# Optimization experiments

Hardware: AMD Instinct MI355X
Metric: run time of the kernel (lower is better)

## Reference

```python
import jax, jax.numpy as jnp
import numpy as np

B, N, C, E, K = 2, 1024, 128, 64, 20

def setup_inputs() -> dict:
    key = jax.random.key(0)
    ks = jax.random.split(key, 4)
    x = jax.random.normal(ks[0], (B, N, C), dtype=jnp.float32)
    Wl = jax.random.normal(ks[1], (C, E), dtype=jnp.float32) * 0.05
    Wr = jax.random.normal(ks[2], (C, E), dtype=jnp.float32) * 0.05
    att = jax.random.normal(ks[3], (1, E), dtype=jnp.float32) * 0.1
    bl = jnp.zeros((E,), dtype=jnp.float32)
    br = jnp.zeros((E,), dtype=jnp.float32)
    edge_index = jnp.zeros((2, 1), dtype=jnp.int64)
    batch = jnp.zeros((B * N,), dtype=jnp.int64)
    return {"x": x, "Wl": Wl, "bl": bl, "Wr": Wr, "br": br, "att": att,
            "edge_index": edge_index, "batch": batch}

def reference(x, Wl, bl, Wr, br, att, edge_index, batch):
    # x: [B, N, C]
    b, n, _ = x.shape
    x_l = x @ Wl + bl              # [B, N, E]
    x_r = x @ Wr + br              # [B, N, E]
    # dense pairwise scores: leaky_relu(x_l_i + x_r_j) . att  -> [B, N, N]
    x_cat = jax.nn.leaky_relu(x_l[:, :, None, :] + x_r[:, None, :, :], 0.2)
    alpha = jnp.einsum('bijd,d->bij', x_cat, att[0])
    alpha = jnp.nan_to_num(alpha, nan=0.0, posinf=0.0, neginf=0.0)
    k = min(K, n)
    vals, idx = jax.lax.top_k(alpha, k)            # [B, N, k]
    attention = jax.nn.softmax(vals, axis=-1).reshape(-1)  # [B*N*k]
    # edge index construction (dropout p used only in training; eval = identity)
    offset = (jnp.arange(b) * n)[:, None]                      # [B, 1]
    index_i = jnp.tile(jnp.repeat(jnp.arange(n), k)[None, :], (b, 1)) + offset
    index_j = idx.reshape(b, n * k) + offset
    new_edge_index = jnp.stack([index_i.reshape(-1), index_j.reshape(-1)], axis=0)
    return new_edge_index, attention
```

## Files before the change

kernel.cpp:

```cpp
#include <hip/hip_runtime.h>

#define Bq 2
#define Nq 1024
#define Cq 128
#define Eq 64
#define Kq 20
#define TI 4
#define BN (Bq * Nq)
#define BNK (BN * Kq)
#define NEGF (-3.0e38f)

#define DPP_F(x, ctrl) __int_as_float(__builtin_amdgcn_update_dpp( \
    __float_as_int(x), __float_as_int(x), (ctrl), 0xf, 0xf, false))
#define DPP_I(x, ctrl) __builtin_amdgcn_update_dpp((x), (x), (ctrl), 0xf, 0xf, false)
#define RL_F(x, l) __int_as_float(__builtin_amdgcn_readlane(__float_as_int(x), (l)))
#define RL_I(x, l) __builtin_amdgcn_readlane((x), (l))
#define QP_XOR1 0xB1
#define QP_XOR2 0x4E
#define ROR4    0x124
#define ROR8    0x128

__global__ __launch_bounds__(128) void proj_kernel(
    const float* __restrict__ x, const float* __restrict__ Wl,
    const float* __restrict__ bl, const float* __restrict__ Wr,
    const float* __restrict__ br, const float* __restrict__ att,
    float* __restrict__ xl, float* __restrict__ xrP, float* __restrict__ rdot) {
  const int row = blockIdx.x;
  const int t = threadIdx.x;
  const int e = t & 63;
  const bool left = (t < 64);
  __shared__ float xs[Cq];
  xs[t] = x[(size_t)row * Cq + t];
  __syncthreads();
  const float* __restrict__ W = left ? Wl : Wr;
  float acc = 0.f;
#pragma unroll 8
  for (int c = 0; c < Cq; ++c) acc = fmaf(xs[c], W[c * Eq + e], acc);
  acc += left ? bl[e] : br[e];
  if (left) {
    xl[(size_t)row * Eq + e] = acc;
  } else {
    xrP[((size_t)(e >> 2) * BN + row) * 4 + (e & 3)] = acc;
    float s = acc * att[e];
    s += DPP_F(s, QP_XOR1);
    s += DPP_F(s, QP_XOR2);
    s += DPP_F(s, ROR4);
    s += DPP_F(s, ROR8);
    const float sd = (RL_F(s, 0) + RL_F(s, 16)) + (RL_F(s, 32) + RL_F(s, 48));
    if (e == 0) rdot[row] = sd;
  }
}

__global__ __launch_bounds__(512) void attn_kernel(
    const float* __restrict__ xl, const float* __restrict__ xrP,
    const float* __restrict__ rdot, const float* __restrict__ att,
    float* __restrict__ out) {
  const int r0g  = blockIdx.x * TI;
  const int b    = r0g >> 10;
  const int tid  = threadIdx.x;
  const int lane = tid & 63;
  const int wave = tid >> 6;

  __shared__ float alpha[TI][Nq];

  {
    const int jt = tid;
    const float* __restrict__ xlw = xl + (size_t)r0g * Eq;

    const float rd0 = 1.5f * rdot[b * Nq + jt];
    const float rd1 = 1.5f * rdot[b * Nq + jt + 512];
    float acc[TI][2];
#pragma unroll
    for (int r = 0; r < TI; ++r) { acc[r][0] = rd0; acc[r][1] = rd1; }

    const float* __restrict__ vb = xrP + (size_t)(b * Nq + jt) * 4;
    float4 nv0 = *(const float4*)(vb);
    float4 nv1 = *(const float4*)(vb + 512 * 4);
    float4 na0 = *(const float4*)(xlw);
    float4 na1 = *(const float4*)(xlw + Eq);
    float4 na2 = *(const float4*)(xlw + 2 * Eq);
    float4 na3 = *(const float4*)(xlw + 3 * Eq);
    float4 nat = *(const float4*)(att);

#pragma unroll
    for (int ch = 0; ch < 16; ++ch) {
      const float4 v0 = nv0, v1 = nv1;
      const float4 a0 = na0, a1 = na1, a2 = na2, a3 = na3, at = nat;
      if (ch < 15) {
        vb += BN * 4;
        nv0 = *(const float4*)(vb);
        nv1 = *(const float4*)(vb + 512 * 4);
        na0 = *(const float4*)(xlw + (ch + 1) * 4);
        na1 = *(const float4*)(xlw + Eq + (ch + 1) * 4);
        na2 = *(const float4*)(xlw + 2 * Eq + (ch + 1) * 4);
        na3 = *(const float4*)(xlw + 3 * Eq + (ch + 1) * 4);
        nat = *(const float4*)(att + (ch + 1) * 4);
      }
      const float* v0p = (const float*)&v0;
      const float* v1p = (const float*)&v1;
      const float* a0p = (const float*)&a0;
      const float* a1p = (const float*)&a1;
      const float* a2p = (const float*)&a2;
      const float* a3p = (const float*)&a3;
      const float* atp = (const float*)&at;
#pragma unroll
      for (int dd = 0; dd < 4; ++dd) {
        const float a = atp[dd];
        const float x0 = v0p[dd], x1 = v1p[dd];
        acc[0][0] = fmaf(fabsf(a0p[dd] + x0), a, acc[0][0]);
        acc[0][1] = fmaf(fabsf(a0p[dd] + x1), a, acc[0][1]);
        acc[1][0] = fmaf(fabsf(a1p[dd] + x0), a, acc[1][0]);
        acc[1][1] = fmaf(fabsf(a1p[dd] + x1), a, acc[1][1]);
        acc[2][0] = fmaf(fabsf(a2p[dd] + x0), a, acc[2][0]);
        acc[2][1] = fmaf(fabsf(a2p[dd] + x1), a, acc[2][1]);
        acc[3][0] = fmaf(fabsf(a3p[dd] + x0), a, acc[3][0]);
        acc[3][1] = fmaf(fabsf(a3p[dd] + x1), a, acc[3][1]);
      }
    }
#pragma unroll
    for (int r = 0; r < TI; ++r) {
      alpha[r][jt]       = acc[r][0];
      alpha[r][jt + 512] = acc[r][1];
    }
  }
  __syncthreads();

  if (wave < TI) {
    float vals[16];
#pragma unroll
    for (int s = 0; s < 16; ++s) vals[s] = alpha[wave][lane + 64 * s];

    float lv = vals[0];
    int   pk = lane;
#pragma unroll
    for (int s = 1; s < 16; ++s)
      if (vals[s] > lv) { lv = vals[s]; pk = (s << 6) | lane; }

    float m0 = 0.f, ssum = 0.f, myv = 0.f;
    int myi = 0;
#pragma unroll 1
    for (int round = 0; round < Kq; ++round) {
      float m = lv;
      m = fmaxf(m, DPP_F(m, QP_XOR1));
      m = fmaxf(m, DPP_F(m, QP_XOR2));
      m = fmaxf(m, DPP_F(m, ROR4));
      m = fmaxf(m, DPP_F(m, ROR8));
      const float bv = fmaxf(fmaxf(RL_F(m, 0), RL_F(m, 16)),
                             fmaxf(RL_F(m, 32), RL_F(m, 48)));
      int key = (lv == bv) ? pk : 0x7FFFFFFF;
      key = min(key, DPP_I(key, QP_XOR1));
      key = min(key, DPP_I(key, QP_XOR2));
      key = min(key, DPP_I(key, ROR4));
      key = min(key, DPP_I(key, ROR8));
      const int jsel = min(min(RL_I(key, 0), RL_I(key, 16)),
                           min(RL_I(key, 32), RL_I(key, 48)));
      if (round == 0) m0 = bv;
      ssum += __expf(0.4f * (bv - m0));
      if (lane == round) { myv = bv; myi = jsel; }
      if (lane == (jsel & 63)) {
        const int sk = jsel >> 6;
#pragma unroll
        for (int s = 0; s < 16; ++s)
          if (s == sk) vals[s] = NEGF;
        lv = vals[0]; pk = lane;
#pragma unroll
        for (int s = 1; s < 16; ++s)
          if (vals[s] > lv) { lv = vals[s]; pk = (s << 6) | lane; }
      }
    }

    if (lane < Kq) {
      const int gi = r0g + wave;
      const float p = __expf(0.4f * (myv - m0)) / ssum;
      const int base = gi * Kq + lane;
      out[base]            = (float)gi;
      out[BNK + base]      = (float)(b * Nq + myi);
      out[2 * BNK + base]  = p;
    }
  }
}

extern "C" void kernel_launch(void* const* d_in, const int* in_sizes, int n_in,
                              void* d_out, int out_size, void* d_ws, size_t ws_size,
                              hipStream_t stream) {
  const float* x   = (const float*)d_in[0];
  const float* Wl  = (const float*)d_in[1];
  const float* bl  = (const float*)d_in[2];
  const float* Wr  = (const float*)d_in[3];
  const float* br  = (const float*)d_in[4];
  const float* att = (const float*)d_in[5];
  float* out = (float*)d_out;

  float* xl   = (float*)d_ws;
  float* xrP  = xl + (size_t)BN * Eq;
  float* rdot = xrP + (size_t)16 * BN * 4;

  proj_kernel<<<BN, 128, 0, stream>>>(x, Wl, bl, Wr, br, att, xl, xrP, rdot);
  attn_kernel<<<BN / TI, 512, 0, stream>>>(xl, xrP, rdot, att, out);
}
```

Measured before the change: 38.78 us.

## Tile eight query rows per block so every wave runs a top-k selection

Each attention block now handles eight rows instead of four, so each xr column load is reused across twice as many rows and all eight waves do top-k work instead of half of them sitting idle. The prefetch changes to a two-deep double buffer over xr planes, and xl/att values are read directly inside the inner loop instead of being preloaded into registers. An occupancy hint of 4 blocks per SM is added. The trade-off is more accumulator registers, twice the LDS for alpha, and half as many blocks.

```diff
diff --git a/kernel.cpp b/kernel.cpp
--- a/kernel.cpp
+++ b/kernel.cpp
@@ -5,7 +5,7 @@
 #define Cq 128
 #define Eq 64
 #define Kq 20
-#define TI 4
+#define TI 8
 #define BN (Bq * Nq)
 #define BNK (BN * Kq)
 #define NEGF (-3.0e38f)
@@ -51,7 +51,7 @@
   }
 }
 
-__global__ __launch_bounds__(512) void attn_kernel(
+__global__ __launch_bounds__(512, 4) void attn_kernel(
     const float* __restrict__ xl, const float* __restrict__ xrP,
     const float* __restrict__ rdot, const float* __restrict__ att,
     float* __restrict__ out) {
@@ -74,47 +74,36 @@
     for (int r = 0; r < TI; ++r) { acc[r][0] = rd0; acc[r][1] = rd1; }
 
     const float* __restrict__ vb = xrP + (size_t)(b * Nq + jt) * 4;
-    float4 nv0 = *(const float4*)(vb);
-    float4 nv1 = *(const float4*)(vb + 512 * 4);
-    float4 na0 = *(const float4*)(xlw);
-    float4 na1 = *(const float4*)(xlw + Eq);
-    float4 na2 = *(const float4*)(xlw + 2 * Eq);
-    float4 na3 = *(const float4*)(xlw + 3 * Eq);
-    float4 nat = *(const float4*)(att);
+    const size_t plane = (size_t)BN * 4;
+
+    float4 va[2], vc[2];
+    va[0] = *(const float4*)(vb);
+    vc[0] = *(const float4*)(vb + 512 * 4);
+    va[1] = *(const float4*)(vb + plane);
+    vc[1] = *(const float4*)(vb + plane + 512 * 4);
 
 #pragma unroll
     for (int ch = 0; ch < 16; ++ch) {
-      const float4 v0 = nv0, v1 = nv1;
-      const float4 a0 = na0, a1 = na1, a2 = na2, a3 = na3, at = nat;
-      if (ch < 15) {
-        vb += BN * 4;
-        nv0 = *(const float4*)(vb);
-        nv1 = *(const float4*)(vb + 512 * 4);
-        na0 = *(const float4*)(xlw + (ch + 1) * 4);
-        na1 = *(const float4*)(xlw + Eq + (ch + 1) * 4);
-        na2 = *(const float4*)(xlw + 2 * Eq + (ch + 1) * 4);
-        na3 = *(const float4*)(xlw + 3 * Eq + (ch + 1) * 4);
-        nat = *(const float4*)(att + (ch + 1) * 4);
+      const float4 v0 = va[ch & 1];
+      const float4 v1 = vc[ch & 1];
+      if (ch < 14) {
+        va[ch & 1] = *(const float4*)(vb + (ch + 2) * plane);
+        vc[ch & 1] = *(const float4*)(vb + (ch + 2) * plane + 512 * 4);
       }
+      const float4 at = *(const float4*)(att + ch * 4);
       const float* v0p = (const float*)&v0;
       const float* v1p = (const float*)&v1;
-      const float* a0p = (const float*)&a0;
-      const float* a1p = (const float*)&a1;
-      const float* a2p = (const float*)&a2;
-      const float* a3p = (const float*)&a3;
       const float* atp = (const float*)&at;
 #pragma unroll
       for (int dd = 0; dd < 4; ++dd) {
         const float a = atp[dd];
         const float x0 = v0p[dd], x1 = v1p[dd];
-        acc[0][0] = fmaf(fabsf(a0p[dd] + x0), a, acc[0][0]);
-        acc[0][1] = fmaf(fabsf(a0p[dd] + x1), a, acc[0][1]);
-        acc[1][0] = fmaf(fabsf(a1p[dd] + x0), a, acc[1][0]);
-        acc[1][1] = fmaf(fabsf(a1p[dd] + x1), a, acc[1][1]);
-        acc[2][0] = fmaf(fabsf(a2p[dd] + x0), a, acc[2][0]);
-        acc[2][1] = fmaf(fabsf(a2p[dd] + x1), a, acc[2][1]);
-        acc[3][0] = fmaf(fabsf(a3p[dd] + x0), a, acc[3][0]);
-        acc[3][1] = fmaf(fabsf(a3p[dd] + x1), a, acc[3][1]);
+#pragma unroll
+        for (int r = 0; r < TI; ++r) {
+          const float xld = xlw[r * Eq + ch * 4 + dd];
+          acc[r][0] = fmaf(fabsf(xld + x0), a, acc[r][0]);
+          acc[r][1] = fmaf(fabsf(xld + x1), a, acc[r][1]);
+        }
       }
     }
 #pragma unroll
@@ -125,7 +114,7 @@
   }
   __syncthreads();
 
-  if (wave < TI) {
+  {
     float vals[16];
 #pragma unroll
     for (int s = 0; s < 16; ++s) vals[s] = alpha[wave][lane + 64 * s];
```

Result: slower. 51.42 us (+32.6%).

## Fuse projection and attention top-k into one cooperative kernel with grid sync

Applied to the files above, without the earlier changes.

Merges the projection kernel and the attention/top-k kernel into a single cooperative launch of 256 blocks. A grid-wide sync separates the projection phase from the attention phase. Each block projects 8 rows, one wave per row computing both the left and right outputs, then runs two 4-row attention groups. This removes one kernel launch and the gap between the two kernels. In exchange it adds a grid barrier and halves the attention-phase parallelism (256 blocks instead of 512), which can leave the GPU underfilled. It also requires all blocks to be co-resident.

```diff
diff --git a/kernel.cpp b/kernel.cpp
--- a/kernel.cpp
+++ b/kernel.cpp
@@ -1,11 +1,13 @@
 #include <hip/hip_runtime.h>
+#include <hip/hip_cooperative_groups.h>
+
+namespace cg = cooperative_groups;
 
 #define Bq 2
 #define Nq 1024
 #define Cq 128
 #define Eq 64
 #define Kq 20
-#define TI 4
 #define BN (Bq * Nq)
 #define BNK (BN * Kq)
 #define NEGF (-3.0e38f)
@@ -20,28 +22,42 @@
 #define ROR4    0x124
 #define ROR8    0x128
 
-__global__ __launch_bounds__(128) void proj_kernel(
+__global__ __launch_bounds__(512) void fused_kernel(
     const float* __restrict__ x, const float* __restrict__ Wl,
     const float* __restrict__ bl, const float* __restrict__ Wr,
     const float* __restrict__ br, const float* __restrict__ att,
-    float* __restrict__ xl, float* __restrict__ xrP, float* __restrict__ rdot) {
-  const int row = blockIdx.x;
-  const int t = threadIdx.x;
-  const int e = t & 63;
-  const bool left = (t < 64);
-  __shared__ float xs[Cq];
-  xs[t] = x[(size_t)row * Cq + t];
+    float* __restrict__ xl, float* __restrict__ xrP, float* __restrict__ rdot,
+    float* __restrict__ out) {
+  const int tid  = threadIdx.x;
+  const int lane = tid & 63;
+  const int wave = tid >> 6;
+
+  __shared__ float xs[8][Cq];
+  __shared__ float alpha[4][Nq];
+
+  {
+    const int idx = tid * 2;
+    const float2 v = *(const float2*)&x[(size_t)blockIdx.x * 8 * Cq + idx];
+    xs[idx >> 7][idx & 127] = v.x;
+    xs[idx >> 7][(idx & 127) + 1] = v.y;
+  }
   __syncthreads();
-  const float* __restrict__ W = left ? Wl : Wr;
-  float acc = 0.f;
+  {
+    const int r = wave;
+    const int e = lane;
+    const int row = blockIdx.x * 8 + r;
+    float accL = 0.f, accR = 0.f;
 #pragma unroll 8
-  for (int c = 0; c < Cq; ++c) acc = fmaf(xs[c], W[c * Eq + e], acc);
-  acc += left ? bl[e] : br[e];
-  if (left) {
-    xl[(size_t)row * Eq + e] = acc;
-  } else {
-    xrP[((size_t)(e >> 2) * BN + row) * 4 + (e & 3)] = acc;
-    float s = acc * att[e];
+    for (int c = 0; c < Cq; ++c) {
+      const float xv = xs[r][c];
+      accL = fmaf(xv, Wl[c * Eq + e], accL);
+      accR = fmaf(xv, Wr[c * Eq + e], accR);
+    }
+    accL += bl[e];
+    accR += br[e];
+    xl[(size_t)row * Eq + e] = accL;
+    xrP[((size_t)(e >> 2) * BN + row) * 4 + (e & 3)] = accR;
+    float s = accR * att[e];
     s += DPP_F(s, QP_XOR1);
     s += DPP_F(s, QP_XOR2);
     s += DPP_F(s, ROR4);
@@ -49,134 +65,130 @@
     const float sd = (RL_F(s, 0) + RL_F(s, 16)) + (RL_F(s, 32) + RL_F(s, 48));
     if (e == 0) rdot[row] = sd;
   }
-}
-
-__global__ __launch_bounds__(512) void attn_kernel(
-    const float* __restrict__ xl, const float* __restrict__ xrP,
-    const float* __restrict__ rdot, const float* __restrict__ att,
-    float* __restrict__ out) {
-  const int r0g  = blockIdx.x * TI;
-  const int b    = r0g >> 10;
-  const int tid  = threadIdx.x;
-  const int lane = tid & 63;
-  const int wave = tid >> 6;
-
-  __shared__ float alpha[TI][Nq];
-
-  {
-    const int jt = tid;
-    const float* __restrict__ xlw = xl + (size_t)r0g * Eq;
-
-    const float rd0 = 1.5f * rdot[b * Nq + jt];
-    const float rd1 = 1.5f * rdot[b * Nq + jt + 512];
-    float acc[TI][2];
-#pragma unroll
-    for (int r = 0; r < TI; ++r) { acc[r][0] = rd0; acc[r][1] = rd1; }
-
-    const float* __restrict__ vb = xrP + (size_t)(b * Nq + jt) * 4;
-    float4 nv0 = *(const float4*)(vb);
-    float4 nv1 = *(const float4*)(vb + 512 * 4);
-    float4 na0 = *(const float4*)(xlw);
-    float4 na1 = *(const float4*)(xlw + Eq);
-    float4 na2 = *(const float4*)(xlw + 2 * Eq);
-    float4 na3 = *(const float4*)(xlw + 3 * Eq);
-    float4 nat = *(const float4*)(att);
-
-#pragma unroll
-    for (int ch = 0; ch < 16; ++ch) {
-      const float4 v0 = nv0, v1 = nv1;
-      const float4 a0 = na0, a1 = na1, a2 = na2, a3 = na3, at = nat;
-      if (ch < 15) {
-        vb += BN * 4;
-        nv0 = *(const float4*)(vb);
-        nv1 = *(const float4*)(vb + 512 * 4);
-        na0 = *(const float4*)(xlw + (ch + 1) * 4);
-        na1 = *(const float4*)(xlw + Eq + (ch + 1) * 4);
-        na2 = *(const float4*)(xlw + 2 * Eq + (ch + 1) * 4);
-        na3 = *(const float4*)(xlw + 3 * Eq + (ch + 1) * 4);
-        nat = *(const float4*)(att + (ch + 1) * 4);
-      }
-      const float* v0p = (const float*)&v0;
-      const float* v1p = (const float*)&v1;
-      const float* a0p = (const float*)&a0;
-      const float* a1p = (const float*)&a1;
-      const float* a2p = (const float*)&a2;
-      const float* a3p = (const float*)&a3;
-      const float* atp = (const float*)&at;
-#pragma unroll
-      for (int dd = 0; dd < 4; ++dd) {
-        const float a = atp[dd];
-        const float x0 = v0p[dd], x1 = v1p[dd];
-        acc[0][0] = fmaf(fabsf(a0p[dd] + x0), a, acc[0][0]);
-        acc[0][1] = fmaf(fabsf(a0p[dd] + x1), a, acc[0][1]);
-        acc[1][0] = fmaf(fabsf(a1p[dd] + x0), a, acc[1][0]);
-        acc[1][1] = fmaf(fabsf(a1p[dd] + x1), a, acc[1][1]);
-        acc[2][0] = fmaf(fabsf(a2p[dd] + x0), a, acc[2][0]);
-        acc[2][1] = fmaf(fabsf(a2p[dd] + x1), a, acc[2][1]);
-        acc[3][0] = fmaf(fabsf(a3p[dd] + x0), a, acc[3][0]);
-        acc[3][1] = fmaf(fabsf(a3p[dd] + x1), a, acc[3][1]);
+
+  cg::this_grid().sync();
+
+#pragma unroll 1
+  for (int g = 0; g < 2; ++g) {
+    const int r0g = blockIdx.x * 8 + g * 4;
+    const int b   = r0g >> 10;
+
+    {
+      const int jt = tid;
+      const float* __restrict__ xlw = xl + (size_t)r0g * Eq;
+
+      const float rd0 = 1.5f * rdot[b * Nq + jt];
+      const float rd1 = 1.5f * rdot[b * Nq + jt + 512];
+      float acc[4][2];
+#pragma unroll
+      for (int r = 0; r < 4; ++r) { acc[r][0] = rd0; acc[r][1] = rd1; }
+
+      const float* __restrict__ vb = xrP + (size_t)(b * Nq + jt) * 4;
+      float4 nv0 = *(const float4*)(vb);
+      float4 nv1 = *(const float4*)(vb + 512 * 4);
+      float4 na0 = *(const float4*)(xlw);
+      float4 na1 = *(const float4*)(xlw + Eq);
+      float4 na2 = *(const float4*)(xlw + 2 * Eq);
+      float4 na3 = *(const float4*)(xlw + 3 * Eq);
+      float4 nat = *(const float4*)(att);
+
+#pragma unroll
+      for (int ch = 0; ch < 16; ++ch) {
+        const float4 v0 = nv0, v1 = nv1;
+        const float4 a0 = na0, a1 = na1, a2 = na2, a3 = na3, at = nat;
+        if (ch < 15) {
+          vb += BN * 4;
+          nv0 = *(const float4*)(vb);
+          nv1 = *(const float4*)(vb + 512 * 4);
+          na0 = *(const float4*)(xlw + (ch + 1) * 4);
+          na1 = *(const float4*)(xlw + Eq + (ch + 1) * 4);
+          na2 = *(const float4*)(xlw + 2 * Eq + (ch + 1) * 4);
+          na3 = *(const float4*)(xlw + 3 * Eq + (ch + 1) * 4);
+          nat = *(const float4*)(att + (ch + 1) * 4);
+        }
+        const float* v0p = (const float*)&v0;
+        const float* v1p = (const float*)&v1;
+        const float* a0p = (const float*)&a0;
+        const float* a1p = (const float*)&a1;
+        const float* a2p = (const float*)&a2;
+        const float* a3p = (const float*)&a3;
+        const float* atp = (const float*)&at;
+#pragma unroll
+        for (int dd = 0; dd < 4; ++dd) {
+          const float a = atp[dd];
+          const float x0 = v0p[dd], x1 = v1p[dd];
+          acc[0][0] = fmaf(fabsf(a0p[dd] + x0), a, acc[0][0]);
+          acc[0][1] = fmaf(fabsf(a0p[dd] + x1), a, acc[0][1]);
+          acc[1][0] = fmaf(fabsf(a1p[dd] + x0), a, acc[1][0]);
+          acc[1][1] = fmaf(fabsf(a1p[dd] + x1), a, acc[1][1]);
+          acc[2][0] = fmaf(fabsf(a2p[dd] + x0), a, acc[2][0]);
+          acc[2][1] = fmaf(fabsf(a2p[dd] + x1), a, acc[2][1]);
+          acc[3][0] = fmaf(fabsf(a3p[dd] + x0), a, acc[3][0]);
+          acc[3][1] = fmaf(fabsf(a3p[dd] + x1), a, acc[3][1]);
+        }
+      }
+#pragma unroll
+      for (int r = 0; r < 4; ++r) {
+        alpha[r][jt]       = acc[r][0];
+        alpha[r][jt + 512] = acc[r][1];
       }
     }
-#pragma unroll
-    for (int r = 0; r < TI; ++r) {
-      alpha[r][jt]       = acc[r][0];
-      alpha[r][jt + 512] = acc[r][1];
+    __syncthreads();
+
+    if (wave < 4) {
+      float vals[16];
+#pragma unroll
+      for (int s = 0; s < 16; ++s) vals[s] = alpha[wave][lane + 64 * s];
+
+      float lv = vals[0];
+      int   pk = lane;
+#pragma unroll
+      for (int s = 1; s < 16; ++s)
+        if (vals[s] > lv) { lv = vals[s]; pk = (s << 6) | lane; }
+
+      float m0 = 0.f, ssum = 0.f, myv = 0.f;
+      int myi = 0;
+#pragma unroll 1
+      for (int round = 0; round < Kq; ++round) {
+        float m = lv;
+        m = fmaxf(m, DPP_F(m, QP_XOR1));
+        m = fmaxf(m, DPP_F(m, QP_XOR2));
+        m = fmaxf(m, DPP_F(m, ROR4));
+        m = fmaxf(m, DPP_F(m, ROR8));
+        const float bv = fmaxf(fmaxf(RL_F(m, 0), RL_F(m, 16)),
+                               fmaxf(RL_F(m, 32), RL_F(m, 48)));
+        int key = (lv == bv) ? pk : 0x7FFFFFFF;
+        key = min(key, DPP_I(key, QP_XOR1));
+        key = min(key, DPP_I(key, QP_XOR2));
+        key = min(key, DPP_I(key, ROR4));
+        key = min(key, DPP_I(key, ROR8));
+        const int jsel = min(min(RL_I(key, 0), RL_I(key, 16)),
+                             min(RL_I(key, 32), RL_I(key, 48)));
+        if (round == 0) m0 = bv;
+        ssum += __expf(0.4f * (bv - m0));
+        if (lane == round) { myv = bv; myi = jsel; }
+        if (lane == (jsel & 63)) {
+          const int sk = jsel >> 6;
+#pragma unroll
+          for (int s = 0; s < 16; ++s)
+            if (s == sk) vals[s] = NEGF;
+          lv = vals[0]; pk = lane;
+#pragma unroll
+          for (int s = 1; s < 16; ++s)
+            if (vals[s] > lv) { lv = vals[s]; pk = (s << 6) | lane; }
+        }
+      }
+
+      if (lane < Kq) {
+        const int gi = r0g + wave;
+        const float p = __expf(0.4f * (myv - m0)) / ssum;
+        const int base = gi * Kq + lane;
+        out[base]            = (float)gi;
+        out[BNK + base]      = (float)(b * Nq + myi);
+        out[2 * BNK + base]  = p;
+      }
     }
-  }
-  __syncthreads();
-
-  if (wave < TI) {
-    float vals[16];
-#pragma unroll
-    for (int s = 0; s < 16; ++s) vals[s] = alpha[wave][lane + 64 * s];
-
-    float lv = vals[0];
-    int   pk = lane;
-#pragma unroll
-    for (int s = 1; s < 16; ++s)
-      if (vals[s] > lv) { lv = vals[s]; pk = (s << 6) | lane; }
-
-    float m0 = 0.f, ssum = 0.f, myv = 0.f;
-    int myi = 0;
-#pragma unroll 1
-    for (int round = 0; round < Kq; ++round) {
-      float m = lv;
-      m = fmaxf(m, DPP_F(m, QP_XOR1));
-      m = fmaxf(m, DPP_F(m, QP_XOR2));
-      m = fmaxf(m, DPP_F(m, ROR4));
-      m = fmaxf(m, DPP_F(m, ROR8));
-      const float bv = fmaxf(fmaxf(RL_F(m, 0), RL_F(m, 16)),
-                             fmaxf(RL_F(m, 32), RL_F(m, 48)));
-      int key = (lv == bv) ? pk : 0x7FFFFFFF;
-      key = min(key, DPP_I(key, QP_XOR1));
-      key = min(key, DPP_I(key, QP_XOR2));
-      key = min(key, DPP_I(key, ROR4));
-      key = min(key, DPP_I(key, ROR8));
-      const int jsel = min(min(RL_I(key, 0), RL_I(key, 16)),
-                           min(RL_I(key, 32), RL_I(key, 48)));
-      if (round == 0) m0 = bv;
-      ssum += __expf(0.4f * (bv - m0));
-      if (lane == round) { myv = bv; myi = jsel; }
-      if (lane == (jsel & 63)) {
-        const int sk = jsel >> 6;
-#pragma unroll
-        for (int s = 0; s < 16; ++s)
-          if (s == sk) vals[s] = NEGF;
-        lv = vals[0]; pk = lane;
-#pragma unroll
-        for (int s = 1; s < 16; ++s)
-          if (vals[s] > lv) { lv = vals[s]; pk = (s << 6) | lane; }
-      }
-    }
-
-    if (lane < Kq) {
-      const int gi = r0g + wave;
-      const float p = __expf(0.4f * (myv - m0)) / ssum;
-      const int base = gi * Kq + lane;
-      out[base]            = (float)gi;
-      out[BNK + base]      = (float)(b * Nq + myi);
-      out[2 * BNK + base]  = p;
-    }
+    __syncthreads();
   }
 }
 
@@ -195,6 +207,8 @@
   float* xrP  = xl + (size_t)BN * Eq;
   float* rdot = xrP + (size_t)16 * BN * 4;
 
-  proj_kernel<<<BN, 128, 0, stream>>>(x, Wl, bl, Wr, br, att, xl, xrP, rdot);
-  attn_kernel<<<BN / TI, 512, 0, stream>>>(xl, xrP, rdot, att, out);
+  void* args[] = {(void*)&x, (void*)&Wl, (void*)&bl, (void*)&Wr, (void*)&br,
+                  (void*)&att, (void*)&xl, (void*)&xrP, (void*)&rdot, (void*)&out};
+  hipLaunchCooperativeKernel((const void*)fused_kernel, dim3(BN / 8), dim3(512),
+                             args, 0, stream);
 }
```

New measurement: 93.51 us. 2.41x slower.
